# Performance work log

Hardware: AMD Instinct MI355X
Metric: run time of the kernel (lower is better)

The kernel has to match this reference:

```python
import jax, jax.numpy as jnp
import numpy as np

B, S, D, U = 32, 4096, 512, 128

def setup_inputs() -> dict:
    key = jax.random.key(0)
    k1, k2, k3, k4, k5 = jax.random.split(key, 5)
    query = jax.random.normal(k1, (B, D), dtype=jnp.float32)
    values = jax.random.normal(k2, (B, S, D), dtype=jnp.float32)
    s = 1.0 / np.sqrt(D)
    W1 = jax.random.normal(k3, (D, U), dtype=jnp.float32) * s
    W2 = jax.random.normal(k4, (D, U), dtype=jnp.float32) * s
    V = jax.random.normal(k5, (U, 1), dtype=jnp.float32) * (1.0 / np.sqrt(U))
    b1 = jnp.zeros((U,), dtype=jnp.float32)
    b2 = jnp.zeros((U,), dtype=jnp.float32)
    bv = jnp.zeros((1,), dtype=jnp.float32)
    return {"query": query, "values": values, "W1": W1, "b1": b1,
            "W2": W2, "b2": b2, "V": V, "bv": bv}

def reference(query, values, W1, b1, W2, b2, V, bv):
    # query: [B, D] -> [B, 1, U]; values: [B, S, D] -> [B, S, U]
    q_proj = (query @ W1 + b1)[:, None, :]                  # [B, 1, U]
    v_proj = jnp.einsum('bsd,du->bsu', values, W2) + b2      # [B, S, U]
    score = jnp.tanh(q_proj + v_proj) @ V + bv               # [B, S, 1]
    attention_weights = jax.nn.softmax(score, axis=1)        # [B, S, 1]
    context_vector = jnp.sum(attention_weights * values, axis=1)  # [B, D]
    return context_vector, attention_weights
```

## Files before the change

### kernel.cpp

```cpp
#include <hip/hip_runtime.h>
#include <math.h>

#define NB 32
#define NS 4096
#define ND 512
#define NU 128
#define RR 32
#define ASTR 520

typedef __bf16 bf16x8 __attribute__((ext_vector_type(8)));
typedef unsigned short u16x8 __attribute__((ext_vector_type(8)));
typedef float f32x4 __attribute__((ext_vector_type(4)));

union FragCvt { u16x8 u; bf16x8 b; };

__device__ inline unsigned short f2bf(float x) {
  union { float f; unsigned u; } v; v.f = x;
  return (unsigned short)((v.u + 0x7FFFu + ((v.u >> 16) & 1u)) >> 16);
}
__device__ inline float bf2f(unsigned int bits16) {
  union { unsigned u; float f; } v; v.u = bits16 << 16;
  return v.f;
}
__device__ inline float fast_tanh(float x) {
  x = fminf(9.f, fmaxf(-9.f, x));
  float e2 = __expf(2.f * x);
  return (e2 - 1.f) * __builtin_amdgcn_rcpf(e2 + 1.f);
}
__device__ inline int bswz(int byte) { return byte ^ (((byte >> 7) & 7) << 4); }

__global__ void prep_qb(const float* __restrict__ q, const float* __restrict__ W1,
                        const float* __restrict__ b1, const float* __restrict__ b2,
                        float* __restrict__ qb) {
  const int bb = blockIdx.x >> 4;
  const int kc = blockIdx.x & 15;
  const int u  = threadIdx.x & 127;
  const int dh = threadIdx.x >> 7;
  const int d0 = kc * 32 + dh * 16;
  const float* qr = q + bb * ND + d0;
  const float* w  = W1 + (size_t)d0 * NU + u;
  float s = (kc == 0 && dh == 0) ? (b1[u] + b2[u]) : 0.f;
  #pragma unroll
  for (int j = 0; j < 16; ++j) s += qr[j] * w[j * NU];
  atomicAdd(qb + bb * NU + u, s);
}

__global__ void prep_w2s(const float* __restrict__ W2, unsigned short* __restrict__ w2s) {
  const int idx = blockIdx.x * 256 + threadIdx.x;
  const int u = idx & 127;
  const int r = idx >> 7;
  const int k = r & 31, kt = r >> 5;
  w2s[kt * 4096 + u * 32 + k] = f2bf(W2[(size_t)(kt * 32 + k) * NU + u]);
}

__global__ __launch_bounds__(256, 3) void fused_attn(
    const float* __restrict__ values,
    const float* __restrict__ qb,
    const unsigned short* __restrict__ w2s,
    const float* __restrict__ V,
    const float* __restrict__ bvp,
    float* __restrict__ wout,
    float* __restrict__ Cacc,
    float* __restrict__ Lacc)
{
  __shared__ unsigned short Alds[RR * ASTR];
  __shared__ unsigned short Blds[2][128 * 32];
  __shared__ float sbuf[4][16];
  __shared__ float wlds[RR];

  const int tid = threadIdx.x;
  const int b = blockIdx.x >> 7;
  const int chunk = blockIdx.x & 127;
  const int s0 = chunk * RR;

  const uint4* w2s4 = (const uint4*)w2s;
  uint4 breg0 = w2s4[tid * 2];
  uint4 breg1 = w2s4[tid * 2 + 1];

  const float* vbase = values + ((size_t)b * NS + s0) * ND;
  #pragma unroll
  for (int ii = 0; ii < 16; ii += 8) {
    float4 v[8];
    #pragma unroll
    for (int j = 0; j < 8; ++j) {
      const int f = tid + 256 * (ii + j);
      v[j] = *(const float4*)(vbase + (f >> 7) * ND + (f & 127) * 4);
    }
    #pragma unroll
    for (int j = 0; j < 8; ++j) {
      const int f = tid + 256 * (ii + j);
      ushort4 pk;
      pk.x = f2bf(v[j].x); pk.y = f2bf(v[j].y); pk.z = f2bf(v[j].z); pk.w = f2bf(v[j].w);
      *(ushort4*)(&Alds[(f >> 7) * ASTR + (f & 127) * 4]) = pk;
    }
  }

  const int wave = tid >> 6, lane = tid & 63;
  const int quad = lane >> 4, lidx = lane & 15;
  const int mtile = wave & 1;
  const int nbase = (wave >> 1) * 64;

  f32x4 acc[4] = {{0.f,0.f,0.f,0.f},{0.f,0.f,0.f,0.f},{0.f,0.f,0.f,0.f},{0.f,0.f,0.f,0.f}};
  const unsigned short* arow = &Alds[(mtile * 16 + lidx) * ASTR];

  for (int kt = 0; kt < 16; ++kt) {
    char* bdst = (char*)Blds[kt & 1];
    const int by0 = tid * 32;
    *(uint4*)(bdst + bswz(by0))      = breg0;
    *(uint4*)(bdst + bswz(by0 + 16)) = breg1;
    __syncthreads();
    if (kt < 15) {
      breg0 = w2s4[(kt + 1) * 512 + tid * 2];
      breg1 = w2s4[(kt + 1) * 512 + tid * 2 + 1];
    }
    FragCvt af; af.u = *(const u16x8*)(arow + kt * 32 + quad * 8);
    const char* bsrc = (const char*)Blds[kt & 1];
    #pragma unroll
    for (int nt = 0; nt < 4; ++nt) {
      const int bb2 = (nbase + nt * 16 + lidx) * 64 + quad * 16;
      FragCvt bf; bf.u = *(const u16x8*)(bsrc + bswz(bb2));
      acc[nt] = __builtin_amdgcn_mfma_f32_16x16x32_bf16(af.b, bf.b, acc[nt], 0, 0, 0);
    }
  }

  float part[4] = {0.f, 0.f, 0.f, 0.f};
  #pragma unroll
  for (int nt = 0; nt < 4; ++nt) {
    const int col = nbase + nt * 16 + lidx;
    const float qv = qb[b * NU + col];
    const float vv = V[col];
    #pragma unroll
    for (int r = 0; r < 4; ++r)
      part[r] += fast_tanh(acc[nt][r] + qv) * vv;
  }
  #pragma unroll
  for (int m = 1; m <= 8; m <<= 1) {
    #pragma unroll
    for (int r = 0; r < 4; ++r) part[r] += __shfl_xor(part[r], m, 64);
  }
  if (lidx == 0) {
    #pragma unroll
    for (int r = 0; r < 4; ++r) sbuf[wave][quad * 4 + r] = part[r];
  }
  __syncthreads();

  if (tid < 32) {
    const int mt = tid >> 4, rr = tid & 15;
    float s = sbuf[mt][rr] + sbuf[mt + 2][rr];
    float e = __expf(s + *bvp);
    wout[(size_t)b * NS + s0 + tid] = e;
    wlds[tid] = e;
    float es = e;
    #pragma unroll
    for (int m = 1; m <= 16; m <<= 1) es += __shfl_xor(es, m, 64);
    if (tid == 0) atomicAdd(Lacc + b, es);
  }
  __syncthreads();

  const int d0 = tid * 2;
  float c0 = 0.f, c1 = 0.f;
  #pragma unroll 8
  for (int r = 0; r < RR; ++r) {
    const float w = wlds[r];
    const unsigned int pk = *(const unsigned int*)(&Alds[r * ASTR + d0]);
    c0 += w * bf2f(pk & 0xFFFFu);
    c1 += w * bf2f(pk >> 16);
  }
  atomicAdd(Cacc + b * ND + d0, c0);
  atomicAdd(Cacc + b * ND + d0 + 1, c1);
}

__global__ void finalize(const float* __restrict__ Cacc, const float* __restrict__ Lacc,
                         float* __restrict__ out) {
  int idx = blockIdx.x * 256 + threadIdx.x;
  if (idx < NB * ND) {
    int b = idx >> 9;
    out[idx] = Cacc[idx] / Lacc[b];
  } else {
    int j = idx - NB * ND;
    int b = j >> 12;
    out[idx] = out[idx] / Lacc[b];
  }
}

extern "C" void kernel_launch(void* const* d_in, const int* in_sizes, int n_in,
                              void* d_out, int out_size, void* d_ws, size_t ws_size,
                              hipStream_t stream) {
  const float* query  = (const float*)d_in[0];
  const float* values = (const float*)d_in[1];
  const float* W1     = (const float*)d_in[2];
  const float* b1     = (const float*)d_in[3];
  const float* W2     = (const float*)d_in[4];
  const float* b2     = (const float*)d_in[5];
  const float* V      = (const float*)d_in[6];
  const float* bv     = (const float*)d_in[7];
  float* out = (float*)d_out;

  char* ws = (char*)d_ws;
  float* Cacc = (float*)ws;
  float* Lacc = (float*)(ws + 65536);
  float* qb   = (float*)(ws + 66048);
  unsigned short* w2s = (unsigned short*)(ws + 66048 + 16384);

  hipMemsetAsync(ws, 0, 66048 + 16384, stream);

  prep_qb <<<NB * 16, 256, 0, stream>>>(query, W1, b1, b2, qb);
  prep_w2s<<<256, 256, 0, stream>>>(W2, w2s);
  fused_attn<<<NB * (NS / RR), 256, 0, stream>>>(values, qb, w2s, V, bv,
                                                 out + NB * ND, Cacc, Lacc);
  finalize<<<(NB * ND + NB * NS) / 256, 256, 0, stream>>>(Cacc, Lacc, out);
}
```

Measured before the change: 412.7 us.

## Double rows per block, give each wave all columns, swizzle A tile in LDS

After: 416.0 us. No clear change (+0.8%).

```diff
diff --git a/kernel.cpp b/kernel.cpp
--- a/kernel.cpp
+++ b/kernel.cpp
@@ -5,8 +5,7 @@
 #define NS 4096
 #define ND 512
 #define NU 128
-#define RR 32
-#define ASTR 520
+#define RR 64
 
 typedef __bf16 bf16x8 __attribute__((ext_vector_type(8)));
 typedef unsigned short u16x8 __attribute__((ext_vector_type(8)));
@@ -28,6 +27,7 @@
   return (e2 - 1.f) * __builtin_amdgcn_rcpf(e2 + 1.f);
 }
 __device__ inline int bswz(int byte) { return byte ^ (((byte >> 7) & 7) << 4); }
+__device__ inline int aswz(int row, int byte) { return row * 1024 + (byte ^ ((row & 7) << 4)); }
 
 __global__ void prep_qb(const float* __restrict__ q, const float* __restrict__ W1,
                         const float* __restrict__ b1, const float* __restrict__ b2,
@@ -53,7 +53,7 @@
   w2s[kt * 4096 + u * 32 + k] = f2bf(W2[(size_t)(kt * 32 + k) * NU + u]);
 }
 
-__global__ __launch_bounds__(256, 3) void fused_attn(
+__global__ __launch_bounds__(256, 2) void fused_attn(
     const float* __restrict__ values,
     const float* __restrict__ qb,
     const unsigned short* __restrict__ w2s,
@@ -63,14 +63,15 @@
     float* __restrict__ Cacc,
     float* __restrict__ Lacc)
 {
-  __shared__ unsigned short Alds[RR * ASTR];
-  __shared__ unsigned short Blds[2][128 * 32];
-  __shared__ float sbuf[4][16];
-  __shared__ float wlds[RR];
+  __shared__ unsigned short Alds[RR * 512];
+  __shared__ union {
+    unsigned short B[2][4096];
+    struct { float sw[64]; float e[64]; } t;
+  } Bsh;
 
   const int tid = threadIdx.x;
-  const int b = blockIdx.x >> 7;
-  const int chunk = blockIdx.x & 127;
+  const int b = blockIdx.x >> 6;
+  const int chunk = blockIdx.x & 63;
   const int s0 = chunk * RR;
 
   const uint4* w2s4 = (const uint4*)w2s;
@@ -78,8 +79,9 @@
   uint4 breg1 = w2s4[tid * 2 + 1];
 
   const float* vbase = values + ((size_t)b * NS + s0) * ND;
-  #pragma unroll
-  for (int ii = 0; ii < 16; ii += 8) {
+  char* Ab = (char*)Alds;
+  #pragma unroll
+  for (int ii = 0; ii < 32; ii += 8) {
     float4 v[8];
     #pragma unroll
     for (int j = 0; j < 8; ++j) {
@@ -89,22 +91,24 @@
     #pragma unroll
     for (int j = 0; j < 8; ++j) {
       const int f = tid + 256 * (ii + j);
+      const int row = f >> 7, c4 = f & 127;
       ushort4 pk;
       pk.x = f2bf(v[j].x); pk.y = f2bf(v[j].y); pk.z = f2bf(v[j].z); pk.w = f2bf(v[j].w);
-      *(ushort4*)(&Alds[(f >> 7) * ASTR + (f & 127) * 4]) = pk;
+      *(ushort4*)(Ab + aswz(row, c4 * 8)) = pk;
     }
   }
 
   const int wave = tid >> 6, lane = tid & 63;
   const int quad = lane >> 4, lidx = lane & 15;
-  const int mtile = wave & 1;
-  const int nbase = (wave >> 1) * 64;
-
-  f32x4 acc[4] = {{0.f,0.f,0.f,0.f},{0.f,0.f,0.f,0.f},{0.f,0.f,0.f,0.f},{0.f,0.f,0.f,0.f}};
-  const unsigned short* arow = &Alds[(mtile * 16 + lidx) * ASTR];
+
+  f32x4 acc[8] = {{0.f,0.f,0.f,0.f},{0.f,0.f,0.f,0.f},{0.f,0.f,0.f,0.f},{0.f,0.f,0.f,0.f},
+                  {0.f,0.f,0.f,0.f},{0.f,0.f,0.f,0.f},{0.f,0.f,0.f,0.f},{0.f,0.f,0.f,0.f}};
+  const int arow = wave * 16 + lidx;
+  const int arswz = (arow & 7) << 4;
+  const char* Arow = Ab + arow * 1024;
 
   for (int kt = 0; kt < 16; ++kt) {
-    char* bdst = (char*)Blds[kt & 1];
+    char* bdst = (char*)Bsh.B[kt & 1];
     const int by0 = tid * 32;
     *(uint4*)(bdst + bswz(by0))      = breg0;
     *(uint4*)(bdst + bswz(by0 + 16)) = breg1;
@@ -113,11 +117,11 @@
       breg0 = w2s4[(kt + 1) * 512 + tid * 2];
       breg1 = w2s4[(kt + 1) * 512 + tid * 2 + 1];
     }
-    FragCvt af; af.u = *(const u16x8*)(arow + kt * 32 + quad * 8);
-    const char* bsrc = (const char*)Blds[kt & 1];
-    #pragma unroll
-    for (int nt = 0; nt < 4; ++nt) {
-      const int bb2 = (nbase + nt * 16 + lidx) * 64 + quad * 16;
+    FragCvt af; af.u = *(const u16x8*)(Arow + ((kt * 64 + quad * 16) ^ arswz));
+    const char* bsrc = (const char*)Bsh.B[kt & 1];
+    #pragma unroll
+    for (int nt = 0; nt < 8; ++nt) {
+      const int bb2 = (nt * 16 + lidx) * 64 + quad * 16;
       FragCvt bf; bf.u = *(const u16x8*)(bsrc + bswz(bb2));
       acc[nt] = __builtin_amdgcn_mfma_f32_16x16x32_bf16(af.b, bf.b, acc[nt], 0, 0, 0);
     }
@@ -125,8 +129,8 @@
 
   float part[4] = {0.f, 0.f, 0.f, 0.f};
   #pragma unroll
-  for (int nt = 0; nt < 4; ++nt) {
-    const int col = nbase + nt * 16 + lidx;
+  for (int nt = 0; nt < 8; ++nt) {
+    const int col = nt * 16 + lidx;
     const float qv = qb[b * NU + col];
     const float vv = V[col];
     #pragma unroll
@@ -140,32 +144,32 @@
   }
   if (lidx == 0) {
     #pragma unroll
-    for (int r = 0; r < 4; ++r) sbuf[wave][quad * 4 + r] = part[r];
+    for (int r = 0; r < 4; ++r) Bsh.t.sw[wave * 16 + quad * 4 + r] = part[r];
   }
   __syncthreads();
 
-  if (tid < 32) {
-    const int mt = tid >> 4, rr = tid & 15;
-    float s = sbuf[mt][rr] + sbuf[mt + 2][rr];
+  if (tid < 64) {
+    float s = Bsh.t.sw[tid];
     float e = __expf(s + *bvp);
     wout[(size_t)b * NS + s0 + tid] = e;
-    wlds[tid] = e;
+    Bsh.t.e[tid] = e;
     float es = e;
     #pragma unroll
-    for (int m = 1; m <= 16; m <<= 1) es += __shfl_xor(es, m, 64);
+    for (int m = 1; m <= 32; m <<= 1) es += __shfl_xor(es, m, 64);
     if (tid == 0) atomicAdd(Lacc + b, es);
   }
   __syncthreads();
 
-  const int d0 = tid * 2;
+  const int d0b = tid * 4;
   float c0 = 0.f, c1 = 0.f;
   #pragma unroll 8
   for (int r = 0; r < RR; ++r) {
-    const float w = wlds[r];
-    const unsigned int pk = *(const unsigned int*)(&Alds[r * ASTR + d0]);
+    const float w = Bsh.t.e[r];
+    const unsigned int pk = *(const unsigned int*)(Ab + aswz(r, d0b));
     c0 += w * bf2f(pk & 0xFFFFu);
     c1 += w * bf2f(pk >> 16);
   }
+  const int d0 = tid * 2;
   atomicAdd(Cacc + b * ND + d0, c0);
   atomicAdd(Cacc + b * ND + d0 + 1, c1);
 }
```
